# Performance work log

Measured on AMD Instinct MI355X. Metric: run time of the kernel, lower is better.

The kernel has to match this reference:

```python
import jax, jax.numpy as jnp
import numpy as np

B = 256       # number of grasp centers (batch)
N = 65536     # total points output by the backbone
C = 1024      # backbone feature channels (enc_channels[-1])
K = 512       # padded slots per segment (points per center)
INFO = 3      # info_size
KCLS = 6      # k_cls
EPS = 1e-5    # LayerNorm eps


def _layernorm(x, g, b):
    m = x.mean(-1, keepdims=True)
    v = ((x - m) ** 2).mean(-1, keepdims=True)
    return (x - m) / jnp.sqrt(v + EPS) * g + b


def setup_inputs() -> dict:
    key = jax.random.key(0)
    ks = jax.random.split(key, 10)
    feat = jax.random.normal(ks[0], (N, C), jnp.float32)
    offsets = jnp.sort(jax.random.randint(ks[1], (B,), 0, N)).astype(jnp.int64)
    offsets = offsets.at[-1].set(N)  # cumulative ends, last covers all points
    info = jax.random.normal(ks[2], (B, INFO), jnp.float32)

    def lin(k, o, i):
        return 0.02 * jax.random.normal(k, (o, i), jnp.float32), jnp.zeros((o,), jnp.float32)

    W1, b1 = lin(ks[3], 512, C)          # point_layer Linear(1024,512)
    Wi, bi = lin(ks[4], 32, INFO)        # info_layer Linear(info_size,32)
    Wa1, ba1 = lin(ks[5], 256, 544)      # anchor_mlp Linear(544,256)
    Wa2, ba2 = lin(ks[6], KCLS, 256)     # anchor_mlp Linear(256,k_cls)
    Wo1, bo1 = lin(ks[7], 256, 544)      # offset_mlp Linear(544,256)
    Wo2, bo2 = lin(ks[8], KCLS * 3, 256) # offset_mlp Linear(256,k_cls*3)
    return dict(
        feat=feat, info=info, offsets=offsets,
        W1=W1, b1=b1, ln1_g=jnp.ones((512,)), ln1_b=jnp.zeros((512,)),
        Wi=Wi, bi=bi,
        Wa1=Wa1, ba1=ba1, lna_g=jnp.ones((256,)), lna_b=jnp.zeros((256,)),
        Wa2=Wa2, ba2=ba2,
        Wo1=Wo1, bo1=bo1, lno_g=jnp.ones((256,)), lno_b=jnp.zeros((256,)),
        Wo2=Wo2, bo2=bo2,
    )


def reference(feat, info, W1, b1, ln1_g, ln1_b, Wi, bi,
              Wa1, ba1, lna_g, lna_b, Wa2, ba2,
              Wo1, bo1, lno_g, lno_b, Wo2, bo2, offsets):
    # --- fused segment-max replaces the pad loop + max over padded dim ---
    # point i belongs to segment b s.t. offsets[b-1] <= i < offsets[b]
    ids = jnp.searchsorted(offsets, jnp.arange(feat.shape[0]), side='right')
    segmax = jax.ops.segment_max(feat, ids, num_segments=B)  # (B, C)
    lengths = jnp.diff(offsets, prepend=0)
    # original zero-pads to K slots: segments shorter than K see 0 in the max
    features = jnp.where((lengths < K)[:, None], jnp.maximum(segmax, 0.0), segmax)

    # point_layer: Linear -> LayerNorm -> Dropout(eval: identity) -> ReLU
    pf = jax.nn.relu(_layernorm(features @ W1.T + b1, ln1_g, ln1_b))
    # info_layer
    inf = info @ Wi.T + bi
    x = jnp.concatenate([pf, inf], axis=1)  # (B, 544)

    pred = jax.nn.relu(_layernorm(x @ Wa1.T + ba1, lna_g, lna_b)) @ Wa2.T + ba2
    off = jax.nn.relu(_layernorm(x @ Wo1.T + bo1, lno_g, lno_b)) @ Wo2.T + bo2
    offset = off.reshape(-1, KCLS, 3)
    return features, pred, offset
```

## Files before the change

kernel.cpp:

```cpp
#include <hip/hip_runtime.h>
#include <hip/hip_bf16.h>
#include <cstdint>

#define NPTS 65536
#define CCH  1024
#define BSEG 256
#define KSLOT 512
#define WROWS 32

typedef float v4f __attribute__((ext_vector_type(4)));

__device__ __forceinline__ unsigned ukey(float f) {
  int i = __float_as_int(f);
  return i >= 0 ? ((unsigned)i | 0x80000000u) : ~(unsigned)i;
}
__device__ __forceinline__ float udec(unsigned u, bool rl) {
  float v;
  if (u >= 0x80000000u) v = __int_as_float((int)(u & 0x7FFFFFFFu));
  else                  v = __int_as_float((int)~u);
  if (u == 0u) v = -__builtin_inff();
  if (rl) v = fmaxf(v, 0.0f);
  return v;
}

__device__ __forceinline__ v4f ntload4(const float* p) {
  return __builtin_nontemporal_load((const v4f*)p);
}
__device__ __forceinline__ v4f vmax4(v4f a, v4f b) {
  v4f r;
  r.x = fmaxf(a.x, b.x); r.y = fmaxf(a.y, b.y);
  r.z = fmaxf(a.z, b.z); r.w = fmaxf(a.w, b.w);
  return r;
}

__global__ __launch_bounds__(256) void segmax_k(const float* __restrict__ feat,
                                                const int* __restrict__ offsets,
                                                unsigned* __restrict__ keys) {
  int t = threadIdx.x;
  int col = t << 2;
  int row0 = blockIdx.x * WROWS;
  int row_end = row0 + WROWS;
  int lo = 0, hi = BSEG - 1;
  while (lo < hi) { int mid = (lo + hi) >> 1; if (offsets[mid] > row0) hi = mid; else lo = mid + 1; }
  int seg = lo;
  int end = offsets[seg];
  const float NI = -__builtin_inff();
  v4f m; m.x = NI; m.y = NI; m.z = NI; m.w = NI;
  bool dirty = false;
  int r = row0;
  while (r < row_end) {
    while (r >= end) {
      if (dirty) {
        unsigned* kp = keys + (size_t)seg * CCH + col;
        atomicMax(kp + 0, ukey(m.x));
        atomicMax(kp + 1, ukey(m.y));
        atomicMax(kp + 2, ukey(m.z));
        atomicMax(kp + 3, ukey(m.w));
        m.x = NI; m.y = NI; m.z = NI; m.w = NI;
        dirty = false;
      }
      ++seg;
      end = offsets[seg];
    }
    int stop = min(row_end, end);
    const float* p = feat + (size_t)r * CCH + col;
    for (; r + 8 <= stop; r += 8) {
      v4f v0 = ntload4(p);
      v4f v1 = ntload4(p + CCH);
      v4f v2 = ntload4(p + 2 * CCH);
      v4f v3 = ntload4(p + 3 * CCH);
      v4f v4 = ntload4(p + 4 * CCH);
      v4f v5 = ntload4(p + 5 * CCH);
      v4f v6 = ntload4(p + 6 * CCH);
      v4f v7 = ntload4(p + 7 * CCH);
      p += 8 * CCH;
      m = vmax4(m, vmax4(vmax4(vmax4(v0, v1), vmax4(v2, v3)),
                         vmax4(vmax4(v4, v5), vmax4(v6, v7))));
    }
    for (; r < stop; ++r) {
      v4f v = ntload4(p);
      p += CCH;
      m = vmax4(m, v);
    }
    dirty = true;
  }
  if (dirty) {
    unsigned* kp = keys + (size_t)seg * CCH + col;
    atomicMax(kp + 0, ukey(m.x));
    atomicMax(kp + 1, ukey(m.y));
    atomicMax(kp + 2, ukey(m.z));
    atomicMax(kp + 3, ukey(m.w));
  }
}

__global__ __launch_bounds__(256) void gemm1_fused(
    const unsigned* __restrict__ keys, const int* __restrict__ offsets,
    const float* __restrict__ W1, float* __restrict__ features,
    float* __restrict__ part) {
  __shared__ float As[32][68];
  __shared__ float Ws[32][68];
  int bx = blockIdx.x, by = blockIdx.y, bz = blockIdx.z;
  int t = threadIdx.x;
  int tx = t & 15, ty = t >> 4;
  int lr = t >> 3;
  int lk = (t & 7) << 2;
  int row0 = by * 64 + lr, row1 = row0 + 32;
  int len0 = offsets[row0] - (row0 ? offsets[row0 - 1] : 0);
  int len1 = offsets[row1] - offsets[row1 - 1];
  bool rl0 = len0 < KSLOT, rl1 = len1 < KSLOT;
  const unsigned* K0 = keys + (size_t)row0 * CCH + lk;
  const unsigned* K1 = keys + (size_t)row1 * CCH + lk;
  int c0 = bx * 64 + lr, c1 = c0 + 32;
  const float* Wr0 = W1 + (size_t)c0 * CCH + lk;
  const float* Wr1 = W1 + (size_t)c1 * CCH + lk;
  float acc[4][4] = {};
  for (int s = 0; s < 8; ++s) {
    int k0 = (bz * 8 + s) << 5;
    uint4 ua = *(const uint4*)(K0 + k0);
    uint4 ub = *(const uint4*)(K1 + k0);
    float4 w0 = *(const float4*)(Wr0 + k0);
    float4 w1 = *(const float4*)(Wr1 + k0);
    float4 a0 = make_float4(udec(ua.x, rl0), udec(ua.y, rl0), udec(ua.z, rl0), udec(ua.w, rl0));
    float4 a1 = make_float4(udec(ub.x, rl1), udec(ub.y, rl1), udec(ub.z, rl1), udec(ub.w, rl1));
    if (bx == 0) {
      *(float4*)(features + (size_t)row0 * CCH + k0 + lk) = a0;
      *(float4*)(features + (size_t)row1 * CCH + k0 + lk) = a1;
    }
    __syncthreads();
    As[lk + 0][lr] = a0.x; As[lk + 1][lr] = a0.y; As[lk + 2][lr] = a0.z; As[lk + 3][lr] = a0.w;
    As[lk + 0][lr + 32] = a1.x; As[lk + 1][lr + 32] = a1.y; As[lk + 2][lr + 32] = a1.z; As[lk + 3][lr + 32] = a1.w;
    Ws[lk + 0][lr] = w0.x; Ws[lk + 1][lr] = w0.y; Ws[lk + 2][lr] = w0.z; Ws[lk + 3][lr] = w0.w;
    Ws[lk + 0][lr + 32] = w1.x; Ws[lk + 1][lr + 32] = w1.y; Ws[lk + 2][lr + 32] = w1.z; Ws[lk + 3][lr + 32] = w1.w;
    __syncthreads();
#pragma unroll
    for (int kk = 0; kk < 32; ++kk) {
      float4 av = *(const float4*)&As[kk][ty << 2];
      float4 wv = *(const float4*)&Ws[kk][tx << 2];
      acc[0][0] += av.x * wv.x; acc[0][1] += av.x * wv.y; acc[0][2] += av.x * wv.z; acc[0][3] += av.x * wv.w;
      acc[1][0] += av.y * wv.x; acc[1][1] += av.y * wv.y; acc[1][2] += av.y * wv.z; acc[1][3] += av.y * wv.w;
      acc[2][0] += av.z * wv.x; acc[2][1] += av.z * wv.y; acc[2][2] += av.z * wv.z; acc[2][3] += av.z * wv.w;
      acc[3][0] += av.w * wv.x; acc[3][1] += av.w * wv.y; acc[3][2] += av.w * wv.z; acc[3][3] += av.w * wv.w;
    }
  }
  float* op = part + (size_t)bz * 131072 + (size_t)(by * 64 + (ty << 2)) * 512 + bx * 64 + (tx << 2);
#pragma unroll
  for (int i = 0; i < 4; ++i) {
    *(float4*)(op + (size_t)i * 512) = make_float4(acc[i][0], acc[i][1], acc[i][2], acc[i][3]);
  }
}

__global__ __launch_bounds__(256) void gemm_nt_part(
    const float* __restrict__ A, int lda,
    const float* __restrict__ Wlo, const float* __restrict__ Whi, int nlo, int ldw,
    float* __restrict__ part, int Ktot, int steps_per_chunk) {
  __shared__ float As[32][68];
  __shared__ float Ws[32][68];
  int bx = blockIdx.x, by = blockIdx.y, bz = blockIdx.z;
  int t = threadIdx.x;
  int tx = t & 15, ty = t >> 4;
  int steps_total = Ktot >> 5;
  int step0 = bz * steps_per_chunk;
  int nsteps = min(steps_per_chunk, steps_total - step0);
  int lr = t >> 3;
  int lk = (t & 7) << 2;
  const float* Arow0 = A + (size_t)(by * 64 + lr) * lda + lk;
  const float* Arow1 = Arow0 + (size_t)32 * lda;
  int c0 = bx * 64 + lr;
  int c1 = c0 + 32;
  const float* Wrow0 = (c0 < nlo ? Wlo + (size_t)c0 * ldw : Whi + (size_t)(c0 - nlo) * ldw) + lk;
  const float* Wrow1 = (c1 < nlo ? Wlo + (size_t)c1 * ldw : Whi + (size_t)(c1 - nlo) * ldw) + lk;
  float acc[4][4] = {};
  for (int s = 0; s < nsteps; ++s) {
    int k0 = (step0 + s) << 5;
    float4 a0 = *(const float4*)(Arow0 + k0);
    float4 a1 = *(const float4*)(Arow1 + k0);
    float4 w0 = *(const float4*)(Wrow0 + k0);
    float4 w1 = *(const float4*)(Wrow1 + k0);
    __syncthreads();
    As[lk + 0][lr] = a0.x; As[lk + 1][lr] = a0.y; As[lk + 2][lr] = a0.z; As[lk + 3][lr] = a0.w;
    As[lk + 0][lr + 32] = a1.x; As[lk + 1][lr + 32] = a1.y; As[lk + 2][lr + 32] = a1.z; As[lk + 3][lr + 32] = a1.w;
    Ws[lk + 0][lr] = w0.x; Ws[lk + 1][lr] = w0.y; Ws[lk + 2][lr] = w0.z; Ws[lk + 3][lr] = w0.w;
    Ws[lk + 0][lr + 32] = w1.x; Ws[lk + 1][lr + 32] = w1.y; Ws[lk + 2][lr + 32] = w1.z; Ws[lk + 3][lr + 32] = w1.w;
    __syncthreads();
#pragma unroll
    for (int kk = 0; kk < 32; ++kk) {
      float4 av = *(const float4*)&As[kk][ty << 2];
      float4 wv = *(const float4*)&Ws[kk][tx << 2];
      acc[0][0] += av.x * wv.x; acc[0][1] += av.x * wv.y; acc[0][2] += av.x * wv.z; acc[0][3] += av.x * wv.w;
      acc[1][0] += av.y * wv.x; acc[1][1] += av.y * wv.y; acc[1][2] += av.y * wv.z; acc[1][3] += av.y * wv.w;
      acc[2][0] += av.z * wv.x; acc[2][1] += av.z * wv.y; acc[2][2] += av.z * wv.z; acc[2][3] += av.z * wv.w;
      acc[3][0] += av.w * wv.x; acc[3][1] += av.w * wv.y; acc[3][2] += av.w * wv.z; acc[3][3] += av.w * wv.w;
    }
  }
  float* op = part + (size_t)bz * 131072 + (size_t)(by * 64 + (ty << 2)) * 512 + bx * 64 + (tx << 2);
#pragma unroll
  for (int i = 0; i < 4; ++i) {
    *(float4*)(op + (size_t)i * 512) = make_float4(acc[i][0], acc[i][1], acc[i][2], acc[i][3]);
  }
}

__global__ __launch_bounds__(256) void ln1_x_k(
    const float* __restrict__ part1, const float* __restrict__ b1,
    const float* __restrict__ g, const float* __restrict__ be,
    const float* __restrict__ info, const float* __restrict__ Wi, const float* __restrict__ bi,
    float* __restrict__ x) {
  int b = blockIdx.x, t = threadIdx.x;
  int wv = t >> 6, ln = t & 63;
  __shared__ float red[2][4];
  __shared__ float stats[2];
  const float* p = part1 + (size_t)b * 512;
  float z0 = b1[t] + p[t] + p[131072 + t] + p[262144 + t] + p[393216 + t];
  int c1 = t + 256;
  float z1 = b1[c1] + p[c1] + p[131072 + c1] + p[262144 + c1] + p[393216 + c1];
  float s = z0 + z1, q = z0 * z0 + z1 * z1;
#pragma unroll
  for (int o = 32; o; o >>= 1) { s += __shfl_down(s, o); q += __shfl_down(q, o); }
  if (ln == 0) { red[0][wv] = s; red[1][wv] = q; }
  __syncthreads();
  if (t == 0) {
    float S = red[0][0] + red[0][1] + red[0][2] + red[0][3];
    float Q = red[1][0] + red[1][1] + red[1][2] + red[1][3];
    float mean = S * (1.f / 512.f);
    float var = Q * (1.f / 512.f) - mean * mean;
    stats[0] = mean; stats[1] = rsqrtf(var + 1e-5f);
  }
  __syncthreads();
  float mean = stats[0], rstd = stats[1];
  x[b * 544 + t]  = fmaxf((z0 - mean) * rstd * g[t]  + be[t],  0.f);
  x[b * 544 + c1] = fmaxf((z1 - mean) * rstd * g[c1] + be[c1], 0.f);
  if (t < 32) {
    float i0 = info[b * 3], i1 = info[b * 3 + 1], i2 = info[b * 3 + 2];
    x[b * 544 + 512 + t] = bi[t] + Wi[t * 3] * i0 + Wi[t * 3 + 1] * i1 + Wi[t * 3 + 2] * i2;
  }
}

__global__ __launch_bounds__(256) void heads_k(
    const float* __restrict__ part2,
    const float* __restrict__ ba1, const float* __restrict__ ga, const float* __restrict__ bea,
    const float* __restrict__ Wa2, const float* __restrict__ ba2,
    const float* __restrict__ bo1, const float* __restrict__ go, const float* __restrict__ beo,
    const float* __restrict__ Wo2, const float* __restrict__ bo2,
    float* __restrict__ outp) {
  int b = blockIdx.x, t = threadIdx.x;
  int wv = t >> 6, ln = t & 63;
  __shared__ float h[512];
  __shared__ float red[4][4];
  __shared__ float stats[4];
  const float* p0 = part2 + (size_t)b * 512;
  const float* p1 = p0 + 131072;
  float za = ba1[t] + p0[t] + p1[t];
  float zo = bo1[t] + p0[256 + t] + p1[256 + t];
  float sa = za, qa = za * za, so = zo, qo = zo * zo;
#pragma unroll
  for (int o = 32; o; o >>= 1) {
    sa += __shfl_down(sa, o); qa += __shfl_down(qa, o);
    so += __shfl_down(so, o); qo += __shfl_down(qo, o);
  }
  if (ln == 0) { red[wv][0] = sa; red[wv][1] = qa; red[wv][2] = so; red[wv][3] = qo; }
  __syncthreads();
  if (t == 0) {
    float Sa = red[0][0] + red[1][0] + red[2][0] + red[3][0];
    float Qa = red[0][1] + red[1][1] + red[2][1] + red[3][1];
    float So = red[0][2] + red[1][2] + red[2][2] + red[3][2];
    float Qo = red[0][3] + red[1][3] + red[2][3] + red[3][3];
    float ma = Sa * (1.f / 256.f), va = Qa * (1.f / 256.f) - ma * ma;
    float mo = So * (1.f / 256.f), vo = Qo * (1.f / 256.f) - mo * mo;
    stats[0] = ma; stats[1] = rsqrtf(va + 1e-5f);
    stats[2] = mo; stats[3] = rsqrtf(vo + 1e-5f);
  }
  __syncthreads();
  h[t]       = fmaxf((za - stats[0]) * stats[1] * ga[t] + bea[t], 0.f);
  h[256 + t] = fmaxf((zo - stats[2]) * stats[3] * go[t] + beo[t], 0.f);
  __syncthreads();
  const float* hh = (wv == 0) ? h : (h + 256);
  const float* W2 = (wv == 0) ? Wa2 : Wo2;
  const float* b2 = (wv == 0) ? ba2 : bo2;
  int o0 = (wv == 0) ? 0 : (wv - 1) * 6;
  int base = (wv == 0) ? (262144 + b * 6) : (263680 + b * 18);
  float h0 = hh[ln], h1 = hh[64 + ln], h2v = hh[128 + ln], h3 = hh[192 + ln];
#pragma unroll
  for (int oo = 0; oo < 6; ++oo) {
    int o = o0 + oo;
    const float* w = W2 + o * 256;
    float pr = h0 * w[ln] + h1 * w[64 + ln] + h2v * w[128 + ln] + h3 * w[192 + ln];
#pragma unroll
    for (int d = 32; d; d >>= 1) pr += __shfl_down(pr, d);
    if (ln == 0) outp[base + o] = pr + b2[o];
  }
}

extern "C" void kernel_launch(void* const* d_in, const int* in_sizes, int n_in,
                              void* d_out, int out_size, void* d_ws, size_t ws_size,
                              hipStream_t stream) {
  const float* feat   = (const float*)d_in[0];
  const float* info   = (const float*)d_in[1];
  const int*   offs   = (const int*)d_in[2];
  const float* W1     = (const float*)d_in[3];
  const float* b1     = (const float*)d_in[4];
  const float* ln1_g  = (const float*)d_in[5];
  const float* ln1_b  = (const float*)d_in[6];
  const float* Wi     = (const float*)d_in[7];
  const float* bi     = (const float*)d_in[8];
  const float* Wa1    = (const float*)d_in[9];
  const float* ba1    = (const float*)d_in[10];
  const float* lna_g  = (const float*)d_in[11];
  const float* lna_b  = (const float*)d_in[12];
  const float* Wa2    = (const float*)d_in[13];
  const float* ba2    = (const float*)d_in[14];
  const float* Wo1    = (const float*)d_in[15];
  const float* bo1    = (const float*)d_in[16];
  const float* lno_g  = (const float*)d_in[17];
  const float* lno_b  = (const float*)d_in[18];
  const float* Wo2    = (const float*)d_in[19];
  const float* bo2    = (const float*)d_in[20];

  char* ws = (char*)d_ws;
  unsigned* keys  = (unsigned*)ws;
  float* part1 = (float*)(ws + (1u << 20));
  float* xbuf  = (float*)(ws + 3u * (1u << 20));
  float* part2 = (float*)(ws + 3u * (1u << 20) + 655360u);
  float* features = (float*)d_out;
  float* outp = (float*)d_out;

  hipMemsetAsync(keys, 0, (size_t)BSEG * CCH * sizeof(unsigned), stream);
  segmax_k<<<dim3(NPTS / WROWS), dim3(256), 0, stream>>>(feat, offs, keys);
  gemm1_fused<<<dim3(8, 4, 4), dim3(256), 0, stream>>>(keys, offs, W1, features, part1);
  ln1_x_k<<<dim3(256), dim3(256), 0, stream>>>(part1, b1, ln1_g, ln1_b, info, Wi, bi, xbuf);
  gemm_nt_part<<<dim3(8, 4, 2), dim3(256), 0, stream>>>(
      xbuf, 544, Wa1, Wo1, 256, 544, part2, 544, 9);
  heads_k<<<dim3(256), dim3(256), 0, stream>>>(
      part2, ba1, lna_g, lna_b, Wa2, ba2, bo1, lno_g, lno_b, Wo2, bo2, outp);
}
```

Before: 104.5 us.

## Fuse all stages into one cooperative kernel with grid-wide syncs

Replaces the memset and five separate kernels with a single cooperative launch of 256 blocks that separates the stages with grid.sync(). This removes per-launch gaps. The segment-max stage now has each block scan 256 rows with 16-deep unrolled plain loads instead of nontemporal ones. Both GEMMs are re-split along K (8 chunks and 6 chunks) so all 256 blocks get work. The trade-off is far fewer blocks streaming the large feature tensor, which may cut achievable memory bandwidth, plus the cost of the grid barriers themselves.

```diff
diff --git a/kernel.cpp b/kernel.cpp
--- a/kernel.cpp
+++ b/kernel.cpp
@@ -1,14 +1,27 @@
 #include <hip/hip_runtime.h>
-#include <hip/hip_bf16.h>
+#include <hip/hip_cooperative_groups.h>
 #include <cstdint>
+
+namespace cg = cooperative_groups;
 
 #define NPTS 65536
 #define CCH  1024
 #define BSEG 256
 #define KSLOT 512
-#define WROWS 32
 
 typedef float v4f __attribute__((ext_vector_type(4)));
+
+struct Params {
+  const float* feat; const float* info; const int* offs;
+  const float* W1; const float* b1; const float* ln1_g; const float* ln1_b;
+  const float* Wi; const float* bi;
+  const float* Wa1; const float* ba1; const float* lna_g; const float* lna_b;
+  const float* Wa2; const float* ba2;
+  const float* Wo1; const float* bo1; const float* lno_g; const float* lno_b;
+  const float* Wo2; const float* bo2;
+  unsigned* keys; float* part1; float* part2; float* xbuf;
+  float* out;
+};
 
 __device__ __forceinline__ unsigned ukey(float f) {
   int i = __float_as_int(f);
@@ -22,10 +35,6 @@
   if (rl) v = fmaxf(v, 0.0f);
   return v;
 }
-
-__device__ __forceinline__ v4f ntload4(const float* p) {
-  return __builtin_nontemporal_load((const v4f*)p);
-}
 __device__ __forceinline__ v4f vmax4(v4f a, v4f b) {
   v4f r;
   r.x = fmaxf(a.x, b.x); r.y = fmaxf(a.y, b.y);
@@ -33,301 +42,284 @@
   return r;
 }
 
-__global__ __launch_bounds__(256) void segmax_k(const float* __restrict__ feat,
-                                                const int* __restrict__ offsets,
-                                                unsigned* __restrict__ keys) {
-  int t = threadIdx.x;
-  int col = t << 2;
-  int row0 = blockIdx.x * WROWS;
-  int row_end = row0 + WROWS;
-  int lo = 0, hi = BSEG - 1;
-  while (lo < hi) { int mid = (lo + hi) >> 1; if (offsets[mid] > row0) hi = mid; else lo = mid + 1; }
-  int seg = lo;
-  int end = offsets[seg];
-  const float NI = -__builtin_inff();
-  v4f m; m.x = NI; m.y = NI; m.z = NI; m.w = NI;
-  bool dirty = false;
-  int r = row0;
-  while (r < row_end) {
-    while (r >= end) {
-      if (dirty) {
-        unsigned* kp = keys + (size_t)seg * CCH + col;
-        atomicMax(kp + 0, ukey(m.x));
-        atomicMax(kp + 1, ukey(m.y));
-        atomicMax(kp + 2, ukey(m.z));
-        atomicMax(kp + 3, ukey(m.w));
-        m.x = NI; m.y = NI; m.z = NI; m.w = NI;
-        dirty = false;
-      }
-      ++seg;
-      end = offsets[seg];
-    }
-    int stop = min(row_end, end);
-    const float* p = feat + (size_t)r * CCH + col;
-    for (; r + 8 <= stop; r += 8) {
-      v4f v0 = ntload4(p);
-      v4f v1 = ntload4(p + CCH);
-      v4f v2 = ntload4(p + 2 * CCH);
-      v4f v3 = ntload4(p + 3 * CCH);
-      v4f v4 = ntload4(p + 4 * CCH);
-      v4f v5 = ntload4(p + 5 * CCH);
-      v4f v6 = ntload4(p + 6 * CCH);
-      v4f v7 = ntload4(p + 7 * CCH);
-      p += 8 * CCH;
-      m = vmax4(m, vmax4(vmax4(vmax4(v0, v1), vmax4(v2, v3)),
-                         vmax4(vmax4(v4, v5), vmax4(v6, v7))));
-    }
-    for (; r < stop; ++r) {
-      v4f v = ntload4(p);
-      p += CCH;
-      m = vmax4(m, v);
-    }
-    dirty = true;
-  }
-  if (dirty) {
-    unsigned* kp = keys + (size_t)seg * CCH + col;
-    atomicMax(kp + 0, ukey(m.x));
-    atomicMax(kp + 1, ukey(m.y));
-    atomicMax(kp + 2, ukey(m.z));
-    atomicMax(kp + 3, ukey(m.w));
-  }
-}
-
-__global__ __launch_bounds__(256) void gemm1_fused(
-    const unsigned* __restrict__ keys, const int* __restrict__ offsets,
-    const float* __restrict__ W1, float* __restrict__ features,
-    float* __restrict__ part) {
+__global__ __launch_bounds__(256) void mega_k(Params P) {
+  cg::grid_group grid = cg::this_grid();
+  const int b = blockIdx.x;
+  const int t = threadIdx.x;
+
   __shared__ float As[32][68];
   __shared__ float Ws[32][68];
-  int bx = blockIdx.x, by = blockIdx.y, bz = blockIdx.z;
-  int t = threadIdx.x;
-  int tx = t & 15, ty = t >> 4;
-  int lr = t >> 3;
-  int lk = (t & 7) << 2;
-  int row0 = by * 64 + lr, row1 = row0 + 32;
-  int len0 = offsets[row0] - (row0 ? offsets[row0 - 1] : 0);
-  int len1 = offsets[row1] - offsets[row1 - 1];
-  bool rl0 = len0 < KSLOT, rl1 = len1 < KSLOT;
-  const unsigned* K0 = keys + (size_t)row0 * CCH + lk;
-  const unsigned* K1 = keys + (size_t)row1 * CCH + lk;
-  int c0 = bx * 64 + lr, c1 = c0 + 32;
-  const float* Wr0 = W1 + (size_t)c0 * CCH + lk;
-  const float* Wr1 = W1 + (size_t)c1 * CCH + lk;
-  float acc[4][4] = {};
-  for (int s = 0; s < 8; ++s) {
-    int k0 = (bz * 8 + s) << 5;
-    uint4 ua = *(const uint4*)(K0 + k0);
-    uint4 ub = *(const uint4*)(K1 + k0);
-    float4 w0 = *(const float4*)(Wr0 + k0);
-    float4 w1 = *(const float4*)(Wr1 + k0);
-    float4 a0 = make_float4(udec(ua.x, rl0), udec(ua.y, rl0), udec(ua.z, rl0), udec(ua.w, rl0));
-    float4 a1 = make_float4(udec(ub.x, rl1), udec(ub.y, rl1), udec(ub.z, rl1), udec(ub.w, rl1));
-    if (bx == 0) {
-      *(float4*)(features + (size_t)row0 * CCH + k0 + lk) = a0;
-      *(float4*)(features + (size_t)row1 * CCH + k0 + lk) = a1;
-    }
-    __syncthreads();
-    As[lk + 0][lr] = a0.x; As[lk + 1][lr] = a0.y; As[lk + 2][lr] = a0.z; As[lk + 3][lr] = a0.w;
-    As[lk + 0][lr + 32] = a1.x; As[lk + 1][lr + 32] = a1.y; As[lk + 2][lr + 32] = a1.z; As[lk + 3][lr + 32] = a1.w;
-    Ws[lk + 0][lr] = w0.x; Ws[lk + 1][lr] = w0.y; Ws[lk + 2][lr] = w0.z; Ws[lk + 3][lr] = w0.w;
-    Ws[lk + 0][lr + 32] = w1.x; Ws[lk + 1][lr + 32] = w1.y; Ws[lk + 2][lr + 32] = w1.z; Ws[lk + 3][lr + 32] = w1.w;
-    __syncthreads();
-#pragma unroll
-    for (int kk = 0; kk < 32; ++kk) {
-      float4 av = *(const float4*)&As[kk][ty << 2];
-      float4 wv = *(const float4*)&Ws[kk][tx << 2];
-      acc[0][0] += av.x * wv.x; acc[0][1] += av.x * wv.y; acc[0][2] += av.x * wv.z; acc[0][3] += av.x * wv.w;
-      acc[1][0] += av.y * wv.x; acc[1][1] += av.y * wv.y; acc[1][2] += av.y * wv.z; acc[1][3] += av.y * wv.w;
-      acc[2][0] += av.z * wv.x; acc[2][1] += av.z * wv.y; acc[2][2] += av.z * wv.z; acc[2][3] += av.z * wv.w;
-      acc[3][0] += av.w * wv.x; acc[3][1] += av.w * wv.y; acc[3][2] += av.w * wv.z; acc[3][3] += av.w * wv.w;
-    }
-  }
-  float* op = part + (size_t)bz * 131072 + (size_t)(by * 64 + (ty << 2)) * 512 + bx * 64 + (tx << 2);
-#pragma unroll
-  for (int i = 0; i < 4; ++i) {
-    *(float4*)(op + (size_t)i * 512) = make_float4(acc[i][0], acc[i][1], acc[i][2], acc[i][3]);
-  }
-}
-
-__global__ __launch_bounds__(256) void gemm_nt_part(
-    const float* __restrict__ A, int lda,
-    const float* __restrict__ Wlo, const float* __restrict__ Whi, int nlo, int ldw,
-    float* __restrict__ part, int Ktot, int steps_per_chunk) {
-  __shared__ float As[32][68];
-  __shared__ float Ws[32][68];
-  int bx = blockIdx.x, by = blockIdx.y, bz = blockIdx.z;
-  int t = threadIdx.x;
-  int tx = t & 15, ty = t >> 4;
-  int steps_total = Ktot >> 5;
-  int step0 = bz * steps_per_chunk;
-  int nsteps = min(steps_per_chunk, steps_total - step0);
-  int lr = t >> 3;
-  int lk = (t & 7) << 2;
-  const float* Arow0 = A + (size_t)(by * 64 + lr) * lda + lk;
-  const float* Arow1 = Arow0 + (size_t)32 * lda;
-  int c0 = bx * 64 + lr;
-  int c1 = c0 + 32;
-  const float* Wrow0 = (c0 < nlo ? Wlo + (size_t)c0 * ldw : Whi + (size_t)(c0 - nlo) * ldw) + lk;
-  const float* Wrow1 = (c1 < nlo ? Wlo + (size_t)c1 * ldw : Whi + (size_t)(c1 - nlo) * ldw) + lk;
-  float acc[4][4] = {};
-  for (int s = 0; s < nsteps; ++s) {
-    int k0 = (step0 + s) << 5;
-    float4 a0 = *(const float4*)(Arow0 + k0);
-    float4 a1 = *(const float4*)(Arow1 + k0);
-    float4 w0 = *(const float4*)(Wrow0 + k0);
-    float4 w1 = *(const float4*)(Wrow1 + k0);
-    __syncthreads();
-    As[lk + 0][lr] = a0.x; As[lk + 1][lr] = a0.y; As[lk + 2][lr] = a0.z; As[lk + 3][lr] = a0.w;
-    As[lk + 0][lr + 32] = a1.x; As[lk + 1][lr + 32] = a1.y; As[lk + 2][lr + 32] = a1.z; As[lk + 3][lr + 32] = a1.w;
-    Ws[lk + 0][lr] = w0.x; Ws[lk + 1][lr] = w0.y; Ws[lk + 2][lr] = w0.z; Ws[lk + 3][lr] = w0.w;
-    Ws[lk + 0][lr + 32] = w1.x; Ws[lk + 1][lr + 32] = w1.y; Ws[lk + 2][lr + 32] = w1.z; Ws[lk + 3][lr + 32] = w1.w;
-    __syncthreads();
-#pragma unroll
-    for (int kk = 0; kk < 32; ++kk) {
-      float4 av = *(const float4*)&As[kk][ty << 2];
-      float4 wv = *(const float4*)&Ws[kk][tx << 2];
-      acc[0][0] += av.x * wv.x; acc[0][1] += av.x * wv.y; acc[0][2] += av.x * wv.z; acc[0][3] += av.x * wv.w;
-      acc[1][0] += av.y * wv.x; acc[1][1] += av.y * wv.y; acc[1][2] += av.y * wv.z; acc[1][3] += av.y * wv.w;
-      acc[2][0] += av.z * wv.x; acc[2][1] += av.z * wv.y; acc[2][2] += av.z * wv.z; acc[2][3] += av.z * wv.w;
-      acc[3][0] += av.w * wv.x; acc[3][1] += av.w * wv.y; acc[3][2] += av.w * wv.z; acc[3][3] += av.w * wv.w;
-    }
-  }
-  float* op = part + (size_t)bz * 131072 + (size_t)(by * 64 + (ty << 2)) * 512 + bx * 64 + (tx << 2);
-#pragma unroll
-  for (int i = 0; i < 4; ++i) {
-    *(float4*)(op + (size_t)i * 512) = make_float4(acc[i][0], acc[i][1], acc[i][2], acc[i][3]);
-  }
-}
-
-__global__ __launch_bounds__(256) void ln1_x_k(
-    const float* __restrict__ part1, const float* __restrict__ b1,
-    const float* __restrict__ g, const float* __restrict__ be,
-    const float* __restrict__ info, const float* __restrict__ Wi, const float* __restrict__ bi,
-    float* __restrict__ x) {
-  int b = blockIdx.x, t = threadIdx.x;
-  int wv = t >> 6, ln = t & 63;
-  __shared__ float red[2][4];
-  __shared__ float stats[2];
-  const float* p = part1 + (size_t)b * 512;
-  float z0 = b1[t] + p[t] + p[131072 + t] + p[262144 + t] + p[393216 + t];
-  int c1 = t + 256;
-  float z1 = b1[c1] + p[c1] + p[131072 + c1] + p[262144 + c1] + p[393216 + c1];
-  float s = z0 + z1, q = z0 * z0 + z1 * z1;
-#pragma unroll
-  for (int o = 32; o; o >>= 1) { s += __shfl_down(s, o); q += __shfl_down(q, o); }
-  if (ln == 0) { red[0][wv] = s; red[1][wv] = q; }
-  __syncthreads();
-  if (t == 0) {
-    float S = red[0][0] + red[0][1] + red[0][2] + red[0][3];
-    float Q = red[1][0] + red[1][1] + red[1][2] + red[1][3];
-    float mean = S * (1.f / 512.f);
-    float var = Q * (1.f / 512.f) - mean * mean;
-    stats[0] = mean; stats[1] = rsqrtf(var + 1e-5f);
-  }
-  __syncthreads();
-  float mean = stats[0], rstd = stats[1];
-  x[b * 544 + t]  = fmaxf((z0 - mean) * rstd * g[t]  + be[t],  0.f);
-  x[b * 544 + c1] = fmaxf((z1 - mean) * rstd * g[c1] + be[c1], 0.f);
-  if (t < 32) {
-    float i0 = info[b * 3], i1 = info[b * 3 + 1], i2 = info[b * 3 + 2];
-    x[b * 544 + 512 + t] = bi[t] + Wi[t * 3] * i0 + Wi[t * 3 + 1] * i1 + Wi[t * 3 + 2] * i2;
-  }
-}
-
-__global__ __launch_bounds__(256) void heads_k(
-    const float* __restrict__ part2,
-    const float* __restrict__ ba1, const float* __restrict__ ga, const float* __restrict__ bea,
-    const float* __restrict__ Wa2, const float* __restrict__ ba2,
-    const float* __restrict__ bo1, const float* __restrict__ go, const float* __restrict__ beo,
-    const float* __restrict__ Wo2, const float* __restrict__ bo2,
-    float* __restrict__ outp) {
-  int b = blockIdx.x, t = threadIdx.x;
-  int wv = t >> 6, ln = t & 63;
-  __shared__ float h[512];
-  __shared__ float red[4][4];
-  __shared__ float stats[4];
-  const float* p0 = part2 + (size_t)b * 512;
-  const float* p1 = p0 + 131072;
-  float za = ba1[t] + p0[t] + p1[t];
-  float zo = bo1[t] + p0[256 + t] + p1[256 + t];
-  float sa = za, qa = za * za, so = zo, qo = zo * zo;
-#pragma unroll
-  for (int o = 32; o; o >>= 1) {
-    sa += __shfl_down(sa, o); qa += __shfl_down(qa, o);
-    so += __shfl_down(so, o); qo += __shfl_down(qo, o);
-  }
-  if (ln == 0) { red[wv][0] = sa; red[wv][1] = qa; red[wv][2] = so; red[wv][3] = qo; }
-  __syncthreads();
-  if (t == 0) {
-    float Sa = red[0][0] + red[1][0] + red[2][0] + red[3][0];
-    float Qa = red[0][1] + red[1][1] + red[2][1] + red[3][1];
-    float So = red[0][2] + red[1][2] + red[2][2] + red[3][2];
-    float Qo = red[0][3] + red[1][3] + red[2][3] + red[3][3];
-    float ma = Sa * (1.f / 256.f), va = Qa * (1.f / 256.f) - ma * ma;
-    float mo = So * (1.f / 256.f), vo = Qo * (1.f / 256.f) - mo * mo;
-    stats[0] = ma; stats[1] = rsqrtf(va + 1e-5f);
-    stats[2] = mo; stats[3] = rsqrtf(vo + 1e-5f);
-  }
-  __syncthreads();
-  h[t]       = fmaxf((za - stats[0]) * stats[1] * ga[t] + bea[t], 0.f);
-  h[256 + t] = fmaxf((zo - stats[2]) * stats[3] * go[t] + beo[t], 0.f);
-  __syncthreads();
-  const float* hh = (wv == 0) ? h : (h + 256);
-  const float* W2 = (wv == 0) ? Wa2 : Wo2;
-  const float* b2 = (wv == 0) ? ba2 : bo2;
-  int o0 = (wv == 0) ? 0 : (wv - 1) * 6;
-  int base = (wv == 0) ? (262144 + b * 6) : (263680 + b * 18);
-  float h0 = hh[ln], h1 = hh[64 + ln], h2v = hh[128 + ln], h3 = hh[192 + ln];
-#pragma unroll
-  for (int oo = 0; oo < 6; ++oo) {
-    int o = o0 + oo;
-    const float* w = W2 + o * 256;
-    float pr = h0 * w[ln] + h1 * w[64 + ln] + h2v * w[128 + ln] + h3 * w[192 + ln];
-#pragma unroll
-    for (int d = 32; d; d >>= 1) pr += __shfl_down(pr, d);
-    if (ln == 0) outp[base + o] = pr + b2[o];
+  __shared__ float hbuf[512];
+  __shared__ float sred[16];
+  __shared__ float sstats[4];
+
+  {
+    unsigned* kp = P.keys + (size_t)b * 1024 + t * 4;
+    *(uint4*)kp = make_uint4(0u, 0u, 0u, 0u);
+  }
+  grid.sync();
+
+  {
+    int col = t << 2;
+    int row0 = b << 8;
+    int row_end = row0 + 256;
+    int lo = 0, hi = BSEG - 1;
+    while (lo < hi) { int mid = (lo + hi) >> 1; if (P.offs[mid] > row0) hi = mid; else lo = mid + 1; }
+    int seg = lo;
+    int end = P.offs[seg];
+    const float NI = -__builtin_inff();
+    v4f m; m.x = NI; m.y = NI; m.z = NI; m.w = NI;
+    bool dirty = false;
+    int r = row0;
+    while (r < row_end) {
+      while (r >= end) {
+        if (dirty) {
+          unsigned* kp = P.keys + (size_t)seg * CCH + col;
+          atomicMax(kp + 0, ukey(m.x));
+          atomicMax(kp + 1, ukey(m.y));
+          atomicMax(kp + 2, ukey(m.z));
+          atomicMax(kp + 3, ukey(m.w));
+          m.x = NI; m.y = NI; m.z = NI; m.w = NI;
+          dirty = false;
+        }
+        ++seg;
+        end = P.offs[seg];
+      }
+      int stop = min(row_end, end);
+      const float* p = P.feat + (size_t)r * CCH + col;
+      for (; r + 16 <= stop; r += 16) {
+        v4f v[16];
+#pragma unroll
+        for (int j = 0; j < 16; ++j) v[j] = *(const v4f*)(p + (size_t)j * CCH);
+        p += 16 * CCH;
+#pragma unroll
+        for (int d = 8; d; d >>= 1)
+#pragma unroll
+          for (int j = 0; j < d; ++j) v[j] = vmax4(v[j], v[j + d]);
+        m = vmax4(m, v[0]);
+      }
+      for (; r < stop; ++r) {
+        v4f v = *(const v4f*)(p);
+        p += CCH;
+        m = vmax4(m, v);
+      }
+      dirty = true;
+    }
+    if (dirty) {
+      unsigned* kp = P.keys + (size_t)seg * CCH + col;
+      atomicMax(kp + 0, ukey(m.x));
+      atomicMax(kp + 1, ukey(m.y));
+      atomicMax(kp + 2, ukey(m.z));
+      atomicMax(kp + 3, ukey(m.w));
+    }
+  }
+  grid.sync();
+
+  {
+    int bx = b & 7, by = (b >> 3) & 3, bz = b >> 5;
+    int tx = t & 15, ty = t >> 4;
+    int lr = t >> 3;
+    int lk = (t & 7) << 2;
+    int row0 = by * 64 + lr, row1 = row0 + 32;
+    int len0 = P.offs[row0] - (row0 ? P.offs[row0 - 1] : 0);
+    int len1 = P.offs[row1] - P.offs[row1 - 1];
+    bool rl0 = len0 < KSLOT, rl1 = len1 < KSLOT;
+    const unsigned* K0 = P.keys + (size_t)row0 * CCH + lk;
+    const unsigned* K1 = P.keys + (size_t)row1 * CCH + lk;
+    int c0 = bx * 64 + lr, c1 = c0 + 32;
+    const float* Wr0 = P.W1 + (size_t)c0 * CCH + lk;
+    const float* Wr1 = P.W1 + (size_t)c1 * CCH + lk;
+    float acc[4][4] = {};
+    for (int s = 0; s < 4; ++s) {
+      int k0 = (bz * 4 + s) << 5;
+      uint4 ua = *(const uint4*)(K0 + k0);
+      uint4 ub = *(const uint4*)(K1 + k0);
+      float4 w0 = *(const float4*)(Wr0 + k0);
+      float4 w1 = *(const float4*)(Wr1 + k0);
+      float4 a0 = make_float4(udec(ua.x, rl0), udec(ua.y, rl0), udec(ua.z, rl0), udec(ua.w, rl0));
+      float4 a1 = make_float4(udec(ub.x, rl1), udec(ub.y, rl1), udec(ub.z, rl1), udec(ub.w, rl1));
+      if (bx == 0) {
+        *(float4*)(P.out + (size_t)row0 * CCH + k0 + lk) = a0;
+        *(float4*)(P.out + (size_t)row1 * CCH + k0 + lk) = a1;
+      }
+      __syncthreads();
+      As[lk + 0][lr] = a0.x; As[lk + 1][lr] = a0.y; As[lk + 2][lr] = a0.z; As[lk + 3][lr] = a0.w;
+      As[lk + 0][lr + 32] = a1.x; As[lk + 1][lr + 32] = a1.y; As[lk + 2][lr + 32] = a1.z; As[lk + 3][lr + 32] = a1.w;
+      Ws[lk + 0][lr] = w0.x; Ws[lk + 1][lr] = w0.y; Ws[lk + 2][lr] = w0.z; Ws[lk + 3][lr] = w0.w;
+      Ws[lk + 0][lr + 32] = w1.x; Ws[lk + 1][lr + 32] = w1.y; Ws[lk + 2][lr + 32] = w1.z; Ws[lk + 3][lr + 32] = w1.w;
+      __syncthreads();
+#pragma unroll
+      for (int kk = 0; kk < 32; ++kk) {
+        float4 av = *(const float4*)&As[kk][ty << 2];
+        float4 wv = *(const float4*)&Ws[kk][tx << 2];
+        acc[0][0] += av.x * wv.x; acc[0][1] += av.x * wv.y; acc[0][2] += av.x * wv.z; acc[0][3] += av.x * wv.w;
+        acc[1][0] += av.y * wv.x; acc[1][1] += av.y * wv.y; acc[1][2] += av.y * wv.z; acc[1][3] += av.y * wv.w;
+        acc[2][0] += av.z * wv.x; acc[2][1] += av.z * wv.y; acc[2][2] += av.z * wv.z; acc[2][3] += av.z * wv.w;
+        acc[3][0] += av.w * wv.x; acc[3][1] += av.w * wv.y; acc[3][2] += av.w * wv.z; acc[3][3] += av.w * wv.w;
+      }
+    }
+    float* op = P.part1 + (size_t)bz * 131072 + (size_t)(by * 64 + (ty << 2)) * 512 + bx * 64 + (tx << 2);
+#pragma unroll
+    for (int i = 0; i < 4; ++i)
+      *(float4*)(op + (size_t)i * 512) = make_float4(acc[i][0], acc[i][1], acc[i][2], acc[i][3]);
+  }
+  grid.sync();
+
+  {
+    int wv = t >> 6, ln = t & 63;
+    const float* p = P.part1 + (size_t)b * 512;
+    float z0 = P.b1[t], z1 = P.b1[t + 256];
+#pragma unroll
+    for (int j = 0; j < 8; ++j) {
+      z0 += p[(size_t)j * 131072 + t];
+      z1 += p[(size_t)j * 131072 + t + 256];
+    }
+    float s = z0 + z1, q = z0 * z0 + z1 * z1;
+#pragma unroll
+    for (int o = 32; o; o >>= 1) { s += __shfl_down(s, o); q += __shfl_down(q, o); }
+    if (ln == 0) { sred[wv] = s; sred[4 + wv] = q; }
+    __syncthreads();
+    if (t == 0) {
+      float S = sred[0] + sred[1] + sred[2] + sred[3];
+      float Q = sred[4] + sred[5] + sred[6] + sred[7];
+      float mean = S * (1.f / 512.f);
+      float var = Q * (1.f / 512.f) - mean * mean;
+      sstats[0] = mean; sstats[1] = rsqrtf(var + 1e-5f);
+    }
+    __syncthreads();
+    float mean = sstats[0], rstd = sstats[1];
+    P.xbuf[b * 544 + t]       = fmaxf((z0 - mean) * rstd * P.ln1_g[t]       + P.ln1_b[t],       0.f);
+    P.xbuf[b * 544 + t + 256] = fmaxf((z1 - mean) * rstd * P.ln1_g[t + 256] + P.ln1_b[t + 256], 0.f);
+    if (t < 32) {
+      float i0 = P.info[b * 3], i1 = P.info[b * 3 + 1], i2 = P.info[b * 3 + 2];
+      P.xbuf[b * 544 + 512 + t] = P.bi[t] + P.Wi[t * 3] * i0 + P.Wi[t * 3 + 1] * i1 + P.Wi[t * 3 + 2] * i2;
+    }
+  }
+  grid.sync();
+
+  if (b < 192) {
+    int bx = b & 7, by = (b >> 3) & 3, bz = b >> 5;
+    int tx = t & 15, ty = t >> 4;
+    int lr = t >> 3;
+    int lk = (t & 7) << 2;
+    int step0 = bz * 3;
+    int nsteps = min(3, 17 - step0);
+    const float* Arow0 = P.xbuf + (size_t)(by * 64 + lr) * 544 + lk;
+    const float* Arow1 = Arow0 + (size_t)32 * 544;
+    int c0 = bx * 64 + lr, c1 = c0 + 32;
+    const float* Wrow0 = (c0 < 256 ? P.Wa1 + (size_t)c0 * 544 : P.Wo1 + (size_t)(c0 - 256) * 544) + lk;
+    const float* Wrow1 = (c1 < 256 ? P.Wa1 + (size_t)c1 * 544 : P.Wo1 + (size_t)(c1 - 256) * 544) + lk;
+    float acc[4][4] = {};
+    for (int s = 0; s < nsteps; ++s) {
+      int k0 = (step0 + s) << 5;
+      float4 a0 = *(const float4*)(Arow0 + k0);
+      float4 a1 = *(const float4*)(Arow1 + k0);
+      float4 w0 = *(const float4*)(Wrow0 + k0);
+      float4 w1 = *(const float4*)(Wrow1 + k0);
+      __syncthreads();
+      As[lk + 0][lr] = a0.x; As[lk + 1][lr] = a0.y; As[lk + 2][lr] = a0.z; As[lk + 3][lr] = a0.w;
+      As[lk + 0][lr + 32] = a1.x; As[lk + 1][lr + 32] = a1.y; As[lk + 2][lr + 32] = a1.z; As[lk + 3][lr + 32] = a1.w;
+      Ws[lk + 0][lr] = w0.x; Ws[lk + 1][lr] = w0.y; Ws[lk + 2][lr] = w0.z; Ws[lk + 3][lr] = w0.w;
+      Ws[lk + 0][lr + 32] = w1.x; Ws[lk + 1][lr + 32] = w1.y; Ws[lk + 2][lr + 32] = w1.z; Ws[lk + 3][lr + 32] = w1.w;
+      __syncthreads();
+#pragma unroll
+      for (int kk = 0; kk < 32; ++kk) {
+        float4 av = *(const float4*)&As[kk][ty << 2];
+        float4 wv = *(const float4*)&Ws[kk][tx << 2];
+        acc[0][0] += av.x * wv.x; acc[0][1] += av.x * wv.y; acc[0][2] += av.x * wv.z; acc[0][3] += av.x * wv.w;
+        acc[1][0] += av.y * wv.x; acc[1][1] += av.y * wv.y; acc[1][2] += av.y * wv.z; acc[1][3] += av.y * wv.w;
+        acc[2][0] += av.z * wv.x; acc[2][1] += av.z * wv.y; acc[2][2] += av.z * wv.z; acc[2][3] += av.z * wv.w;
+        acc[3][0] += av.w * wv.x; acc[3][1] += av.w * wv.y; acc[3][2] += av.w * wv.z; acc[3][3] += av.w * wv.w;
+      }
+    }
+    float* op = P.part2 + (size_t)bz * 131072 + (size_t)(by * 64 + (ty << 2)) * 512 + bx * 64 + (tx << 2);
+#pragma unroll
+    for (int i = 0; i < 4; ++i)
+      *(float4*)(op + (size_t)i * 512) = make_float4(acc[i][0], acc[i][1], acc[i][2], acc[i][3]);
+  }
+  grid.sync();
+
+  {
+    int wv = t >> 6, ln = t & 63;
+    const float* p0 = P.part2 + (size_t)b * 512;
+    float za = P.ba1[t], zo = P.bo1[t];
+#pragma unroll
+    for (int j = 0; j < 6; ++j) {
+      za += p0[(size_t)j * 131072 + t];
+      zo += p0[(size_t)j * 131072 + 256 + t];
+    }
+    float sa = za, qa = za * za, so = zo, qo = zo * zo;
+#pragma unroll
+    for (int o = 32; o; o >>= 1) {
+      sa += __shfl_down(sa, o); qa += __shfl_down(qa, o);
+      so += __shfl_down(so, o); qo += __shfl_down(qo, o);
+    }
+    if (ln == 0) { sred[wv] = sa; sred[4 + wv] = qa; sred[8 + wv] = so; sred[12 + wv] = qo; }
+    __syncthreads();
+    if (t == 0) {
+      float Sa = sred[0] + sred[1] + sred[2] + sred[3];
+      float Qa = sred[4] + sred[5] + sred[6] + sred[7];
+      float So = sred[8] + sred[9] + sred[10] + sred[11];
+      float Qo = sred[12] + sred[13] + sred[14] + sred[15];
+      float ma = Sa * (1.f / 256.f), va = Qa * (1.f / 256.f) - ma * ma;
+      float mo = So * (1.f / 256.f), vo = Qo * (1.f / 256.f) - mo * mo;
+      sstats[0] = ma; sstats[1] = rsqrtf(va + 1e-5f);
+      sstats[2] = mo; sstats[3] = rsqrtf(vo + 1e-5f);
+    }
+    __syncthreads();
+    hbuf[t]       = fmaxf((za - sstats[0]) * sstats[1] * P.lna_g[t] + P.lna_b[t], 0.f);
+    hbuf[256 + t] = fmaxf((zo - sstats[2]) * sstats[3] * P.lno_g[t] + P.lno_b[t], 0.f);
+    __syncthreads();
+    const float* hh = (wv == 0) ? hbuf : (hbuf + 256);
+    const float* W2 = (wv == 0) ? P.Wa2 : P.Wo2;
+    const float* b2 = (wv == 0) ? P.ba2 : P.bo2;
+    int o0 = (wv == 0) ? 0 : (wv - 1) * 6;
+    int base = (wv == 0) ? (262144 + b * 6) : (263680 + b * 18);
+    float h0 = hh[ln], h1 = hh[64 + ln], h2v = hh[128 + ln], h3 = hh[192 + ln];
+#pragma unroll
+    for (int oo = 0; oo < 6; ++oo) {
+      int o = o0 + oo;
+      const float* w = W2 + o * 256;
+      float pr = h0 * w[ln] + h1 * w[64 + ln] + h2v * w[128 + ln] + h3 * w[192 + ln];
+#pragma unroll
+      for (int d = 32; d; d >>= 1) pr += __shfl_down(pr, d);
+      if (ln == 0) P.out[base + o] = pr + b2[o];
+    }
   }
 }
 
 extern "C" void kernel_launch(void* const* d_in, const int* in_sizes, int n_in,
                               void* d_out, int out_size, void* d_ws, size_t ws_size,
                               hipStream_t stream) {
-  const float* feat   = (const float*)d_in[0];
-  const float* info   = (const float*)d_in[1];
-  const int*   offs   = (const int*)d_in[2];
-  const float* W1     = (const float*)d_in[3];
-  const float* b1     = (const float*)d_in[4];
-  const float* ln1_g  = (const float*)d_in[5];
-  const float* ln1_b  = (const float*)d_in[6];
-  const float* Wi     = (const float*)d_in[7];
-  const float* bi     = (const float*)d_in[8];
-  const float* Wa1    = (const float*)d_in[9];
-  const float* ba1    = (const float*)d_in[10];
-  const float* lna_g  = (const float*)d_in[11];
-  const float* lna_b  = (const float*)d_in[12];
-  const float* Wa2    = (const float*)d_in[13];
-  const float* ba2    = (const float*)d_in[14];
-  const float* Wo1    = (const float*)d_in[15];
-  const float* bo1    = (const float*)d_in[16];
-  const float* lno_g  = (const float*)d_in[17];
-  const float* lno_b  = (const float*)d_in[18];
-  const float* Wo2    = (const float*)d_in[19];
-  const float* bo2    = (const float*)d_in[20];
-
   char* ws = (char*)d_ws;
-  unsigned* keys  = (unsigned*)ws;
-  float* part1 = (float*)(ws + (1u << 20));
-  float* xbuf  = (float*)(ws + 3u * (1u << 20));
-  float* part2 = (float*)(ws + 3u * (1u << 20) + 655360u);
-  float* features = (float*)d_out;
-  float* outp = (float*)d_out;
-
-  hipMemsetAsync(keys, 0, (size_t)BSEG * CCH * sizeof(unsigned), stream);
-  segmax_k<<<dim3(NPTS / WROWS), dim3(256), 0, stream>>>(feat, offs, keys);
-  gemm1_fused<<<dim3(8, 4, 4), dim3(256), 0, stream>>>(keys, offs, W1, features, part1);
-  ln1_x_k<<<dim3(256), dim3(256), 0, stream>>>(part1, b1, ln1_g, ln1_b, info, Wi, bi, xbuf);
-  gemm_nt_part<<<dim3(8, 4, 2), dim3(256), 0, stream>>>(
-      xbuf, 544, Wa1, Wo1, 256, 544, part2, 544, 9);
-  heads_k<<<dim3(256), dim3(256), 0, stream>>>(
-      part2, ba1, lna_g, lna_b, Wa2, ba2, bo1, lno_g, lno_b, Wo2, bo2, outp);
-}
+  Params P;
+  P.feat  = (const float*)d_in[0];
+  P.info  = (const float*)d_in[1];
+  P.offs  = (const int*)d_in[2];
+  P.W1    = (const float*)d_in[3];
+  P.b1    = (const float*)d_in[4];
+  P.ln1_g = (const float*)d_in[5];
+  P.ln1_b = (const float*)d_in[6];
+  P.Wi    = (const float*)d_in[7];
+  P.bi    = (const float*)d_in[8];
+  P.Wa1   = (const float*)d_in[9];
+  P.ba1   = (const float*)d_in[10];
+  P.lna_g = (const float*)d_in[11];
+  P.lna_b = (const float*)d_in[12];
+  P.Wa2   = (const float*)d_in[13];
+  P.ba2   = (const float*)d_in[14];
+  P.Wo1   = (const float*)d_in[15];
+  P.bo1   = (const float*)d_in[16];
+  P.lno_g = (const float*)d_in[17];
+  P.lno_b = (const float*)d_in[18];
+  P.Wo2   = (const float*)d_in[19];
+  P.bo2   = (const float*)d_in[20];
+  P.part1 = (float*)(ws);
+  P.part2 = (float*)(ws + (4u << 20));
+  P.xbuf  = (float*)(ws + (7u << 20));
+  P.keys  = (unsigned*)(ws + (8u << 20));
+  P.out   = (float*)d_out;
+
+  void* args[] = { &P };
+  hipLaunchCooperativeKernel(mega_k, dim3(256), dim3(256), args, 0, stream);
+}
```

Result: slower. 231.6 us (+121.6%).
